# Kernel tuning notes

Hardware: AMD Instinct MI355X
Metric: run time of the kernel (lower is better)

Reference implementation:

```python
import jax, jax.numpy as jnp
import numpy as np

EPS = 1e-5

def _ln(x):
    # F.layer_norm over last dim, no affine params
    m = jnp.mean(x, axis=-1, keepdims=True)
    v = jnp.mean((x - m) ** 2, axis=-1, keepdims=True)
    return (x - m) * jax.lax.rsqrt(v + EPS)

def _jagged_to_padded(vals, offsets, B, n):
    # vals: [T, F] -> [B, n, F], zero padded
    T = vals.shape[0]
    lengths = offsets[1:] - offsets[:-1]            # [B]
    pos = jnp.arange(n)
    idx = offsets[:-1, None] + pos[None, :]         # [B, n]
    valid = pos[None, :] < lengths[:, None]         # [B, n]
    gathered = vals[jnp.clip(idx, 0, T - 1)]        # [B, n, F]
    return jnp.where(valid[..., None], gathered, 0.0)

def _dense_to_jagged(padded, offsets, T):
    # padded: [B, n, F] -> [T, F]
    t = jnp.arange(T)
    b = jnp.clip(jnp.searchsorted(offsets, t, side='right') - 1, 0, offsets.shape[0] - 2)
    pos = t - offsets[b]
    return padded[b, pos]

def setup_inputs() -> dict:
    key = jax.random.key(0)
    D, H, d = 1024, 8, 128
    B, n = 4, 2048
    T = B * n  # all sequences full length
    ks = jax.random.split(key, 4)
    x = jax.random.normal(ks[0], (T, D), dtype=jnp.float32)
    attnmask = jnp.tril(jnp.ones((n, n), dtype=jnp.float32))
    x_offsets = jnp.arange(B + 1, dtype=jnp.int32) * n
    proj_w = jax.random.normal(ks[1], (D, H * d * 4), dtype=jnp.float32) * 0.02
    out_w = jax.random.normal(ks[2], (H * d, D), dtype=jnp.float32) * 0.02
    out_b = jnp.zeros((D,), dtype=jnp.float32)
    return {"x": x, "attnmask": attnmask, "proj_w": proj_w, "out_w": out_w,
            "out_b": out_b, "x_offsets": x_offsets, "B": B, "n": n}

def reference(x, attnmask, proj_w, out_w, out_b, x_offsets, B, n):
    T, D = x.shape
    H, d4 = 8, proj_w.shape[1] // 8
    d = d4 // 4
    x = _ln(x)
    h = jax.nn.silu(x @ proj_w).reshape(T, H, 4 * d)   # silu BEFORE split (HSTU)
    u, v, q, k = jnp.split(h, 4, axis=-1)              # each [T, H, d]
    pq = _jagged_to_padded(q.reshape(T, H * d), x_offsets, B, n).reshape(B, n, H, d)
    pk = _jagged_to_padded(k.reshape(T, H * d), x_offsets, B, n).reshape(B, n, H, d)
    pv = _jagged_to_padded(v.reshape(T, H * d), x_offsets, B, n).reshape(B, n, H, d)
    scores = jnp.einsum('bnhd,bmhd->bhnm', pq, pk)
    scores = jax.nn.silu(scores) / n * attnmask[None, None]
    attnout = jnp.einsum('bhnm,bmhd->bnhd', scores, pv).reshape(B, n, H * d)
    attnout = _dense_to_jagged(attnout, x_offsets, T)  # [T, H*d]
    attnout = _ln(attnout) * u.reshape(T, H * d)       # fused norm + gate
    return attnout @ out_w + out_b                      # out_proj (dropout inactive: eval)
```

## Files before the change

### kernel.cpp

```cpp
#include <hip/hip_runtime.h>

typedef short  s16x8 __attribute__((ext_vector_type(8)));
typedef float  f32x4 __attribute__((ext_vector_type(4)));
typedef unsigned short u16;
typedef unsigned int   u32;

#define T_TOK 8192
#define D_IN  1024
#define D4    4096
#define NH    8
#define DH    128
#define NSEQ  2048

__device__ __forceinline__ float u16f(u16 s){
  union { unsigned int u; float f; } c; c.u = ((unsigned int)s) << 16; return c.f;
}
__device__ __forceinline__ u16 f2u16(float f){
  union { float f; unsigned int u; } c; c.f = f;
  unsigned int r = (c.u + 0x7fffu + ((c.u >> 16) & 1u)) >> 16;
  return (u16)r;
}
__device__ __forceinline__ unsigned int cvt2_bf16(float a, float b){
  unsigned int r;
  asm("v_cvt_pk_bf16_f32 %0, %1, %2" : "=v"(r) : "v"(a), "v"(b));
  return r;
}
__device__ __forceinline__ float fast_silu(float v){
  return v * __builtin_amdgcn_rcpf(1.0f + __expf(-v));
}
__device__ __forceinline__ void gload_lds16(const u16* g, u16* lds){
  __builtin_amdgcn_global_load_lds(
      (const __attribute__((address_space(1))) u32*)g,
      (__attribute__((address_space(3))) u32*)lds, 16, 0, 0);
}

__device__ __forceinline__ void block_reduce2(float& a, float& b){
  __shared__ float red[8];
  #pragma unroll
  for (int off = 32; off > 0; off >>= 1){
    a += __shfl_down(a, off, 64);
    b += __shfl_down(b, off, 64);
  }
  int w = threadIdx.x >> 6;
  if ((threadIdx.x & 63) == 0){ red[w*2] = a; red[w*2+1] = b; }
  __syncthreads();
  a = red[0] + red[2] + red[4] + red[6];
  b = red[1] + red[3] + red[5] + red[7];
  __syncthreads();
}

__global__ void ln_x_kernel(const float* __restrict__ x, u16* __restrict__ xn){
  int t = blockIdx.x;
  const float* row = x + (size_t)t * D_IN;
  int base = threadIdx.x * 4;
  float4 v = *(const float4*)(row + base);
  float s = v.x + v.y + v.z + v.w;
  float q = v.x*v.x + v.y*v.y + v.z*v.z + v.w*v.w;
  block_reduce2(s, q);
  float mean = s * (1.0f / D_IN);
  float var  = q * (1.0f / D_IN) - mean * mean;
  float rstd = rsqrtf(var + 1e-5f);
  ushort4 o;
  o.x = f2u16((v.x - mean) * rstd); o.y = f2u16((v.y - mean) * rstd);
  o.z = f2u16((v.z - mean) * rstd); o.w = f2u16((v.w - mean) * rstd);
  *(ushort4*)(xn + (size_t)t * D_IN + base) = o;
}

__global__ void transpose_kernel(const float* __restrict__ in, u16* __restrict__ out,
                                 int R, int C){
  __shared__ u16 tile[32][33];
  int c0 = blockIdx.x * 32, r0 = blockIdx.y * 32;
  for (int i = threadIdx.y; i < 32; i += 8)
    tile[i][threadIdx.x] = f2u16(in[(size_t)(r0 + i) * C + c0 + threadIdx.x]);
  __syncthreads();
  for (int i = threadIdx.y; i < 32; i += 8)
    out[(size_t)(c0 + i) * R + r0 + threadIdx.x] = tile[threadIdx.x][i];
}

__global__ void vt_kernel(const u16* __restrict__ h, u16* __restrict__ vt){
  __shared__ u16 tile[32][33];
  int bh = blockIdx.z; int b = bh >> 3, hh = bh & 7;
  int p0 = blockIdx.x * 32, d0 = blockIdx.y * 32;
  const u16* src = h + (size_t)(b * NSEQ) * D4 + hh * 512 + 128;
  for (int i = threadIdx.y; i < 32; i += 8)
    tile[i][threadIdx.x] = src[(size_t)(p0 + i) * D4 + d0 + threadIdx.x];
  __syncthreads();
  u16* dst = vt + (size_t)bh * DH * NSEQ;
  for (int i = threadIdx.y; i < 32; i += 8)
    dst[(size_t)(d0 + i) * NSEQ + p0 + threadIdx.x] = tile[threadIdx.x][i];
}

template<int EPI>
__global__ __launch_bounds__(256, 2) void gemm_bt_kernel(
    const u16* __restrict__ A, const u16* __restrict__ Bt,
    const float* __restrict__ bias, u16* __restrict__ Cb, float* __restrict__ Cf,
    int M, int N, int K)
{
  __shared__ __align__(16) u16 As[128 * 64];
  __shared__ __align__(16) u16 Bs[128 * 64];
  int bn = blockIdx.x, bm = blockIdx.y;
  int tid = threadIdx.x;
  int lane = tid & 63, wave = tid >> 6;
  int lr = lane & 15, quad = lane >> 4;
  int wm = (wave >> 1) * 64, wn = (wave & 1) * 64;
  f32x4 acc[4][4] = {};

  int srow = lane >> 3;
  int scol = ((lane & 7) ^ srow) * 8;
  const u16* Ab = A  + (size_t)(bm * 128) * K;
  const u16* Bb = Bt + (size_t)(bn * 128) * K;
  int swz = (lr & 7) * 8;

  for (int k0 = 0; k0 < K; k0 += 64){
    #pragma unroll
    for (int it = 0; it < 4; ++it){
      int c = it * 4 + wave;
      gload_lds16(Ab + (size_t)(c * 8 + srow) * K + k0 + scol, As + c * 512);
    }
    #pragma unroll
    for (int it = 0; it < 4; ++it){
      int c = it * 4 + wave;
      gload_lds16(Bb + (size_t)(c * 8 + srow) * K + k0 + scol, Bs + c * 512);
    }
    __syncthreads();
    #pragma unroll
    for (int ks = 0; ks < 2; ++ks){
      s16x8 af[4], bf[4];
      #pragma unroll
      for (int i = 0; i < 4; ++i)
        af[i] = *(const s16x8*)&As[(wm + i*16 + lr) * 64 + (((ks*32 + quad*8)) ^ swz)];
      #pragma unroll
      for (int j = 0; j < 4; ++j)
        bf[j] = *(const s16x8*)&Bs[(wn + j*16 + lr) * 64 + (((ks*32 + quad*8)) ^ swz)];
      #pragma unroll
      for (int i = 0; i < 4; ++i)
        #pragma unroll
        for (int j = 0; j < 4; ++j)
          acc[i][j] = __builtin_amdgcn_mfma_f32_16x16x32_bf16(af[i], bf[j], acc[i][j], 0, 0, 0);
    }
    __syncthreads();
  }
  #pragma unroll
  for (int j = 0; j < 4; ++j){
    int nc = bn * 128 + wn + j * 16 + lr;
    float bv = 0.0f;
    if (EPI == 1) bv = bias[nc];
    #pragma unroll
    for (int i = 0; i < 4; ++i){
      #pragma unroll
      for (int r = 0; r < 4; ++r){
        int mr = bm * 128 + wm + i * 16 + quad * 4 + r;
        float v = acc[i][j][r];
        if (EPI == 0){
          v = fast_silu(v);
          Cb[(size_t)mr * N + nc] = f2u16(v);
        } else {
          Cf[(size_t)mr * N + nc] = v + bv;
        }
      }
    }
  }
}

__global__ __launch_bounds__(256, 2) void attn_kernel(
    const u16* __restrict__ h, const u16* __restrict__ vt, u16* __restrict__ ao)
{
  __shared__ __align__(16) u16 smem[40960];

  int id = blockIdx.x;
  int qt, bh;
  if (id < 256) { qt = id & 15;        bh = id >> 4;          }
  else          { qt = 15 - (id & 15); bh = 16 + ((id - 256) >> 4); }
  int b = bh >> 3, hh = bh & 7;
  int tid = threadIdx.x;
  int lane = tid & 63, wave = tid >> 6;
  int lr = lane & 15, quad = lane >> 4;
  int wq = wave * 32;

  const u16* kbase = h  + (size_t)(b * NSEQ) * D4 + hh * 512 + 384;
  const u16* vbase = vt + (size_t)bh * DH * NSEQ;
  u16* Ssl = smem + 32768;

  auto stage = [&](int bufsel, int k0n){
    u16* kd = smem + bufsel * 8192;
    u16* vd = smem + 16384 + bufsel * 8192;
    #pragma unroll
    for (int it = 0; it < 4; ++it){
      int c = it * 4 + wave;
      int row = c * 4 + (lane >> 4);
      int ss = (lane & 15) ^ (row & 15);
      gload_lds16(kbase + (size_t)(k0n + row) * D4 + ss * 8, kd + c * 512);
    }
    #pragma unroll
    for (int it = 0; it < 4; ++it){
      int c = it * 4 + wave;
      int row = c * 8 + (lane >> 3);
      int ss = (lane & 7) ^ (lane >> 3);
      gload_lds16(vbase + (size_t)row * NSEQ + k0n + ss * 8, vd + c * 512);
    }
  };

  const u16* qsrc = h + (size_t)(b * NSEQ + qt * 128) * D4 + hh * 512 + 256;
  s16x8 qf[2][4];
  #pragma unroll
  for (int i = 0; i < 2; ++i)
    #pragma unroll
    for (int ks = 0; ks < 4; ++ks)
      qf[i][ks] = *(const s16x8*)(qsrc + (size_t)(wq + i*16 + lr) * D4 + ks*32 + quad*8);

  stage(0, 0);
  __syncthreads();

  f32x4 oacc[2][8] = {};
  int nkt = 2 * qt + 2;

  for (int kt = 0; kt < nkt; ++kt){
    int cur = kt & 1;
    int k0 = kt * 64;
    if (kt + 1 < nkt) stage(cur ^ 1, k0 + 64);

    const u16* kc = smem + cur * 8192;
    const u16* vc = smem + 16384 + cur * 8192;

    int lk0 = k0 - qt * 128;
    bool active = (lk0 < wq + 32);
    if (active){
      f32x4 sacc[2][4] = {};
      __builtin_amdgcn_s_setprio(1);
      #pragma unroll
      for (int ks = 0; ks < 4; ++ks){
        s16x8 kf[4];
        #pragma unroll
        for (int jb = 0; jb < 4; ++jb)
          kf[jb] = *(const s16x8*)&kc[(jb*16 + lr) * 128 + (((ks*4 + quad) ^ lr) << 3)];
        #pragma unroll
        for (int i = 0; i < 2; ++i)
          #pragma unroll
          for (int jb = 0; jb < 4; ++jb)
            sacc[i][jb] = __builtin_amdgcn_mfma_f32_16x16x32_bf16(qf[i][ks], kf[jb], sacc[i][jb], 0, 0, 0);
      }
      __builtin_amdgcn_s_setprio(0);

      bool needmask = (lk0 + 63 > wq);
      #pragma unroll
      for (int i = 0; i < 2; ++i)
        #pragma unroll
        for (int jb = 0; jb < 4; ++jb){
          int qbase = wq + i*16 + quad*4;
          int slot = jb*2 + (lr >> 3);
          int off  = lr & 7;
          float p[4];
          if (needmask){
            #pragma unroll
            for (int r = 0; r < 4; ++r){
              float v = fast_silu(sacc[i][jb][r]);
              if (lk0 + jb*16 + lr > qbase + r) v = 0.0f;
              p[r] = v;
            }
          } else {
            #pragma unroll
            for (int r = 0; r < 4; ++r)
              p[r] = fast_silu(sacc[i][jb][r]);
          }
          unsigned int c01 = cvt2_bf16(p[0], p[1]);
          unsigned int c23 = cvt2_bf16(p[2], p[3]);
          Ssl[(qbase+0)*64 + (((slot ^ ((qbase+0)&7)) << 3) | off)] = (u16)(c01);
          Ssl[(qbase+1)*64 + (((slot ^ ((qbase+1)&7)) << 3) | off)] = (u16)(c01 >> 16);
          Ssl[(qbase+2)*64 + (((slot ^ ((qbase+2)&7)) << 3) | off)] = (u16)(c23);
          Ssl[(qbase+3)*64 + (((slot ^ ((qbase+3)&7)) << 3) | off)] = (u16)(c23 >> 16);
        }

      __builtin_amdgcn_s_setprio(1);
      #pragma unroll
      for (int ks = 0; ks < 2; ++ks){
        s16x8 pf[2], vf2[8];
        #pragma unroll
        for (int i = 0; i < 2; ++i)
          pf[i] = *(const s16x8*)&Ssl[(wq + i*16 + lr) * 64 + (((ks*4 + quad) ^ (lr & 7)) << 3)];
        #pragma unroll
        for (int j = 0; j < 8; ++j)
          vf2[j] = *(const s16x8*)&vc[(j*16 + lr) * 64 + (((ks*4 + quad) ^ (lr & 7)) << 3)];
        #pragma unroll
        for (int i = 0; i < 2; ++i)
          #pragma unroll
          for (int j = 0; j < 8; ++j)
            oacc[i][j] = __builtin_amdgcn_mfma_f32_16x16x32_bf16(pf[i], vf2[j], oacc[i][j], 0, 0, 0);
      }
      __builtin_amdgcn_s_setprio(0);
    }
    __syncthreads();
  }

  u16* aobase = ao + (size_t)(b * NSEQ + qt * 128) * D_IN + hh * DH;
  #pragma unroll
  for (int i = 0; i < 2; ++i)
    #pragma unroll
    for (int j = 0; j < 8; ++j){
      float s0 = oacc[i][j][0] * (1.0f / (float)NSEQ);
      float s1 = oacc[i][j][1] * (1.0f / (float)NSEQ);
      float s2 = oacc[i][j][2] * (1.0f / (float)NSEQ);
      float s3 = oacc[i][j][3] * (1.0f / (float)NSEQ);
      unsigned int c01 = cvt2_bf16(s0, s1);
      unsigned int c23 = cvt2_bf16(s2, s3);
      int rbase = wq + i*16 + quad*4;
      aobase[(size_t)(rbase+0) * D_IN + j*16 + lr] = (u16)(c01);
      aobase[(size_t)(rbase+1) * D_IN + j*16 + lr] = (u16)(c01 >> 16);
      aobase[(size_t)(rbase+2) * D_IN + j*16 + lr] = (u16)(c23);
      aobase[(size_t)(rbase+3) * D_IN + j*16 + lr] = (u16)(c23 >> 16);
    }
}

__global__ void ln_gate_kernel(const u16* __restrict__ ao, const u16* __restrict__ h,
                               u16* __restrict__ gated){
  int t = blockIdx.x;
  const u16* row = ao + (size_t)t * D_IN;
  int base = threadIdx.x * 4;
  ushort4 raw = *(const ushort4*)(row + base);
  float vx = u16f(raw.x), vy = u16f(raw.y), vz = u16f(raw.z), vw = u16f(raw.w);
  float s = vx + vy + vz + vw;
  float q = vx*vx + vy*vy + vz*vz + vw*vw;
  block_reduce2(s, q);
  float mean = s * (1.0f / D_IN);
  float var  = q * (1.0f / D_IN) - mean * mean;
  float rstd = rsqrtf(var + 1e-5f);
  ushort4 uu = *(const ushort4*)(h + (size_t)t * D4 + (base >> 7) * 512 + (base & 127));
  ushort4 o;
  o.x = f2u16((vx - mean) * rstd * u16f(uu.x));
  o.y = f2u16((vy - mean) * rstd * u16f(uu.y));
  o.z = f2u16((vz - mean) * rstd * u16f(uu.z));
  o.w = f2u16((vw - mean) * rstd * u16f(uu.w));
  *(ushort4*)(gated + (size_t)t * D_IN + base) = o;
}

extern "C" void kernel_launch(void* const* d_in, const int* in_sizes, int n_in,
                              void* d_out, int out_size, void* d_ws, size_t ws_size,
                              hipStream_t stream)
{
  (void)in_sizes; (void)n_in; (void)out_size; (void)ws_size;
  const float* x      = (const float*)d_in[0];
  const float* proj_w = (const float*)d_in[2];
  const float* out_w  = (const float*)d_in[3];
  const float* out_b  = (const float*)d_in[4];
  float* out = (float*)d_out;

  const size_t MB = 1024 * 1024;
  char* ws = (char*)d_ws;
  u16* xn  = (u16*)(ws);
  u16* h   = (u16*)(ws + 16 * MB);
  u16* Wt  = (u16*)(ws + 80 * MB);
  u16* OWt = (u16*)(ws + 88 * MB);
  u16* Vt  = (u16*)(ws + 90 * MB);
  u16* ao    = xn;
  u16* gated = Vt;

  dim3 tb32(32, 8);
  hipLaunchKernelGGL(transpose_kernel, dim3(D4 / 32, D_IN / 32), tb32, 0, stream,
                     proj_w, Wt, D_IN, D4);
  hipLaunchKernelGGL(transpose_kernel, dim3(D_IN / 32, D_IN / 32), tb32, 0, stream,
                     out_w, OWt, D_IN, D_IN);
  hipLaunchKernelGGL(ln_x_kernel, dim3(T_TOK), dim3(256), 0, stream, x, xn);
  hipLaunchKernelGGL(HIP_KERNEL_NAME(gemm_bt_kernel<0>), dim3(D4 / 128, T_TOK / 128),
                     dim3(256), 0, stream, xn, Wt, (const float*)nullptr, h,
                     (float*)nullptr, T_TOK, D4, D_IN);
  hipLaunchKernelGGL(vt_kernel, dim3(NSEQ / 32, DH / 32, 32), tb32, 0, stream, h, Vt);
  hipLaunchKernelGGL(attn_kernel, dim3(512), dim3(256), 0, stream, h, Vt, ao);
  hipLaunchKernelGGL(ln_gate_kernel, dim3(T_TOK), dim3(256), 0, stream, ao, h, gated);
  hipLaunchKernelGGL(HIP_KERNEL_NAME(gemm_bt_kernel<1>), dim3(D_IN / 128, T_TOK / 128),
                     dim3(256), 0, stream, gated, OWt, out_b, (u16*)nullptr,
                     out, T_TOK, D_IN, D_IN);
}
```

Before: 319.4 us.

## Split attention query tile across 8 waves of 16 rows each

The attention kernel moves from 4 waves handling 32 query rows each to 8 waves (512 threads) handling 16 rows each, with cooperative K/V staging split over 8 waves. The goal is more waves resident per CU to hide latency, and finer causal skipping per wave. In exchange, each wave reuses every K/V fragment loaded from LDS for only one query row-block instead of two, which raises LDS read traffic per MFMA. Launch bounds also move to (512,4), which may limit registers.

```diff
diff --git a/kernel.cpp b/kernel.cpp
--- a/kernel.cpp
+++ b/kernel.cpp
@@ -162,7 +162,7 @@
   }
 }
 
-__global__ __launch_bounds__(256, 2) void attn_kernel(
+__global__ __launch_bounds__(512, 4) void attn_kernel(
     const u16* __restrict__ h, const u16* __restrict__ vt, u16* __restrict__ ao)
 {
   __shared__ __align__(16) u16 smem[40960];
@@ -175,7 +175,7 @@
   int tid = threadIdx.x;
   int lane = tid & 63, wave = tid >> 6;
   int lr = lane & 15, quad = lane >> 4;
-  int wq = wave * 32;
+  int wq = wave * 16;
 
   const u16* kbase = h  + (size_t)(b * NSEQ) * D4 + hh * 512 + 384;
   const u16* vbase = vt + (size_t)bh * DH * NSEQ;
@@ -185,15 +185,15 @@
     u16* kd = smem + bufsel * 8192;
     u16* vd = smem + 16384 + bufsel * 8192;
     #pragma unroll
-    for (int it = 0; it < 4; ++it){
-      int c = it * 4 + wave;
+    for (int it = 0; it < 2; ++it){
+      int c = it * 8 + wave;
       int row = c * 4 + (lane >> 4);
       int ss = (lane & 15) ^ (row & 15);
       gload_lds16(kbase + (size_t)(k0n + row) * D4 + ss * 8, kd + c * 512);
     }
     #pragma unroll
-    for (int it = 0; it < 4; ++it){
-      int c = it * 4 + wave;
+    for (int it = 0; it < 2; ++it){
+      int c = it * 8 + wave;
       int row = c * 8 + (lane >> 3);
       int ss = (lane & 7) ^ (lane >> 3);
       gload_lds16(vbase + (size_t)row * NSEQ + k0n + ss * 8, vd + c * 512);
@@ -201,17 +201,15 @@
   };
 
   const u16* qsrc = h + (size_t)(b * NSEQ + qt * 128) * D4 + hh * 512 + 256;
-  s16x8 qf[2][4];
+  s16x8 qf[4];
   #pragma unroll
-  for (int i = 0; i < 2; ++i)
-    #pragma unroll
-    for (int ks = 0; ks < 4; ++ks)
-      qf[i][ks] = *(const s16x8*)(qsrc + (size_t)(wq + i*16 + lr) * D4 + ks*32 + quad*8);
+  for (int ks = 0; ks < 4; ++ks)
+    qf[ks] = *(const s16x8*)(qsrc + (size_t)(wq + lr) * D4 + ks*32 + quad*8);
 
   stage(0, 0);
   __syncthreads();
 
-  f32x4 oacc[2][8] = {};
+  f32x4 oacc[8] = {};
   int nkt = 2 * qt + 2;
 
   for (int kt = 0; kt < nkt; ++kt){
@@ -223,9 +221,9 @@
     const u16* vc = smem + 16384 + cur * 8192;
 
     int lk0 = k0 - qt * 128;
-    bool active = (lk0 < wq + 32);
+    bool active = (lk0 < wq + 16);
     if (active){
-      f32x4 sacc[2][4] = {};
+      f32x4 sacc[4] = {};
       __builtin_amdgcn_s_setprio(1);
       #pragma unroll
       for (int ks = 0; ks < 4; ++ks){
@@ -234,57 +232,49 @@
         for (int jb = 0; jb < 4; ++jb)
           kf[jb] = *(const s16x8*)&kc[(jb*16 + lr) * 128 + (((ks*4 + quad) ^ lr) << 3)];
         #pragma unroll
-        for (int i = 0; i < 2; ++i)
-          #pragma unroll
-          for (int jb = 0; jb < 4; ++jb)
-            sacc[i][jb] = __builtin_amdgcn_mfma_f32_16x16x32_bf16(qf[i][ks], kf[jb], sacc[i][jb], 0, 0, 0);
+        for (int jb = 0; jb < 4; ++jb)
+          sacc[jb] = __builtin_amdgcn_mfma_f32_16x16x32_bf16(qf[ks], kf[jb], sacc[jb], 0, 0, 0);
       }
       __builtin_amdgcn_s_setprio(0);
 
       bool needmask = (lk0 + 63 > wq);
       #pragma unroll
-      for (int i = 0; i < 2; ++i)
-        #pragma unroll
-        for (int jb = 0; jb < 4; ++jb){
-          int qbase = wq + i*16 + quad*4;
-          int slot = jb*2 + (lr >> 3);
-          int off  = lr & 7;
-          float p[4];
-          if (needmask){
-            #pragma unroll
-            for (int r = 0; r < 4; ++r){
-              float v = fast_silu(sacc[i][jb][r]);
-              if (lk0 + jb*16 + lr > qbase + r) v = 0.0f;
-              p[r] = v;
-            }
-          } else {
-            #pragma unroll
-            for (int r = 0; r < 4; ++r)
-              p[r] = fast_silu(sacc[i][jb][r]);
+      for (int jb = 0; jb < 4; ++jb){
+        int qbase = wq + quad*4;
+        int slot = jb*2 + (lr >> 3);
+        int off  = lr & 7;
+        float p[4];
+        if (needmask){
+          #pragma unroll
+          for (int r = 0; r < 4; ++r){
+            float v = fast_silu(sacc[jb][r]);
+            if (lk0 + jb*16 + lr > qbase + r) v = 0.0f;
+            p[r] = v;
           }
-          unsigned int c01 = cvt2_bf16(p[0], p[1]);
-          unsigned int c23 = cvt2_bf16(p[2], p[3]);
-          Ssl[(qbase+0)*64 + (((slot ^ ((qbase+0)&7)) << 3) | off)] = (u16)(c01);
-          Ssl[(qbase+1)*64 + (((slot ^ ((qbase+1)&7)) << 3) | off)] = (u16)(c01 >> 16);
-          Ssl[(qbase+2)*64 + (((slot ^ ((qbase+2)&7)) << 3) | off)] = (u16)(c23);
-          Ssl[(qbase+3)*64 + (((slot ^ ((qbase+3)&7)) << 3) | off)] = (u16)(c23 >> 16);
+        } else {
+          #pragma unroll
+          for (int r = 0; r < 4; ++r)
+            p[r] = fast_silu(sacc[jb][r]);
         }
+        unsigned int c01 = cvt2_bf16(p[0], p[1]);
+        unsigned int c23 = cvt2_bf16(p[2], p[3]);
+        Ssl[(qbase+0)*64 + (((slot ^ ((qbase+0)&7)) << 3) | off)] = (u16)(c01);
+        Ssl[(qbase+1)*64 + (((slot ^ ((qbase+1)&7)) << 3) | off)] = (u16)(c01 >> 16);
+        Ssl[(qbase+2)*64 + (((slot ^ ((qbase+2)&7)) << 3) | off)] = (u16)(c23);
+        Ssl[(qbase+3)*64 + (((slot ^ ((qbase+3)&7)) << 3) | off)] = (u16)(c23 >> 16);
+      }
 
       __builtin_amdgcn_s_setprio(1);
       #pragma unroll
       for (int ks = 0; ks < 2; ++ks){
-        s16x8 pf[2], vf2[8];
-        #pragma unroll
-        for (int i = 0; i < 2; ++i)
-          pf[i] = *(const s16x8*)&Ssl[(wq + i*16 + lr) * 64 + (((ks*4 + quad) ^ (lr & 7)) << 3)];
+        s16x8 pf, vf2[8];
+        pf = *(const s16x8*)&Ssl[(wq + lr) * 64 + (((ks*4 + quad) ^ (lr & 7)) << 3)];
         #pragma unroll
         for (int j = 0; j < 8; ++j)
           vf2[j] = *(const s16x8*)&vc[(j*16 + lr) * 64 + (((ks*4 + quad) ^ (lr & 7)) << 3)];
         #pragma unroll
-        for (int i = 0; i < 2; ++i)
-          #pragma unroll
-          for (int j = 0; j < 8; ++j)
-            oacc[i][j] = __builtin_amdgcn_mfma_f32_16x16x32_bf16(pf[i], vf2[j], oacc[i][j], 0, 0, 0);
+        for (int j = 0; j < 8; ++j)
+          oacc[j] = __builtin_amdgcn_mfma_f32_16x16x32_bf16(pf, vf2[j], oacc[j], 0, 0, 0);
       }
       __builtin_amdgcn_s_setprio(0);
     }
@@ -293,21 +283,19 @@
 
   u16* aobase = ao + (size_t)(b * NSEQ + qt * 128) * D_IN + hh * DH;
   #pragma unroll
-  for (int i = 0; i < 2; ++i)
-    #pragma unroll
-    for (int j = 0; j < 8; ++j){
-      float s0 = oacc[i][j][0] * (1.0f / (float)NSEQ);
-      float s1 = oacc[i][j][1] * (1.0f / (float)NSEQ);
-      float s2 = oacc[i][j][2] * (1.0f / (float)NSEQ);
-      float s3 = oacc[i][j][3] * (1.0f / (float)NSEQ);
-      unsigned int c01 = cvt2_bf16(s0, s1);
-      unsigned int c23 = cvt2_bf16(s2, s3);
-      int rbase = wq + i*16 + quad*4;
-      aobase[(size_t)(rbase+0) * D_IN + j*16 + lr] = (u16)(c01);
-      aobase[(size_t)(rbase+1) * D_IN + j*16 + lr] = (u16)(c01 >> 16);
-      aobase[(size_t)(rbase+2) * D_IN + j*16 + lr] = (u16)(c23);
-      aobase[(size_t)(rbase+3) * D_IN + j*16 + lr] = (u16)(c23 >> 16);
-    }
+  for (int j = 0; j < 8; ++j){
+    float s0 = oacc[j][0] * (1.0f / (float)NSEQ);
+    float s1 = oacc[j][1] * (1.0f / (float)NSEQ);
+    float s2 = oacc[j][2] * (1.0f / (float)NSEQ);
+    float s3 = oacc[j][3] * (1.0f / (float)NSEQ);
+    unsigned int c01 = cvt2_bf16(s0, s1);
+    unsigned int c23 = cvt2_bf16(s2, s3);
+    int rbase = wq + quad*4;
+    aobase[(size_t)(rbase+0) * D_IN + j*16 + lr] = (u16)(c01);
+    aobase[(size_t)(rbase+1) * D_IN + j*16 + lr] = (u16)(c01 >> 16);
+    aobase[(size_t)(rbase+2) * D_IN + j*16 + lr] = (u16)(c23);
+    aobase[(size_t)(rbase+3) * D_IN + j*16 + lr] = (u16)(c23 >> 16);
+  }
 }
 
 __global__ void ln_gate_kernel(const u16* __restrict__ ao, const u16* __restrict__ h,
@@ -363,7 +351,7 @@
                      dim3(256), 0, stream, xn, Wt, (const float*)nullptr, h,
                      (float*)nullptr, T_TOK, D4, D_IN);
   hipLaunchKernelGGL(vt_kernel, dim3(NSEQ / 32, DH / 32, 32), tb32, 0, stream, h, Vt);
-  hipLaunchKernelGGL(attn_kernel, dim3(512), dim3(256), 0, stream, h, Vt, ao);
+  hipLaunchKernelGGL(attn_kernel, dim3(512), dim3(512), 0, stream, h, Vt, ao);
   hipLaunchKernelGGL(ln_gate_kernel, dim3(T_TOK), dim3(256), 0, stream, ao, h, gated);
   hipLaunchKernelGGL(HIP_KERNEL_NAME(gemm_bt_kernel<1>), dim3(D_IN / 128, T_TOK / 128),
                      dim3(256), 0, stream, gated, OWt, out_b, (u16*)nullptr,
```

Result: faster. 311.1 us (-2.6%).

## Split attention key tiles across two wave groups and reduce partial outputs

Applied to the files above, without the earlier changes.

The attention block grows to 512 threads in two groups of four waves. Each group handles alternating 64-key tiles with its own double-buffered K/V staging, and the P tile now reuses the K buffer instead of a separate slice. At the end, group 1's partial outputs go through shared memory and group 0 adds them before writing. The aim is more waves per block to hide latency and halve the serial key loop, at the cost of 128KB of LDS (lower occupancy), an extra mid-loop barrier and a final reduction.

```diff
diff --git a/kernel.cpp b/kernel.cpp
--- a/kernel.cpp
+++ b/kernel.cpp
@@ -162,10 +162,10 @@
   }
 }
 
-__global__ __launch_bounds__(256, 2) void attn_kernel(
+__global__ __launch_bounds__(512, 2) void attn_kernel(
     const u16* __restrict__ h, const u16* __restrict__ vt, u16* __restrict__ ao)
 {
-  __shared__ __align__(16) u16 smem[40960];
+  __shared__ __align__(16) u16 smem[65536];
 
   int id = blockIdx.x;
   int qt, bh;
@@ -174,26 +174,27 @@
   int b = bh >> 3, hh = bh & 7;
   int tid = threadIdx.x;
   int lane = tid & 63, wave = tid >> 6;
+  int g = wave >> 2, w4 = wave & 3;
   int lr = lane & 15, quad = lane >> 4;
-  int wq = wave * 32;
+  int wq = w4 * 32;
 
   const u16* kbase = h  + (size_t)(b * NSEQ) * D4 + hh * 512 + 384;
   const u16* vbase = vt + (size_t)bh * DH * NSEQ;
-  u16* Ssl = smem + 32768;
-
-  auto stage = [&](int bufsel, int k0n){
-    u16* kd = smem + bufsel * 8192;
-    u16* vd = smem + 16384 + bufsel * 8192;
+
+  auto stage = [&](int d, int t){
+    u16* kd = smem + (size_t)(g*2 + d) * 8192;
+    u16* vd = smem + 32768 + (size_t)(g*2 + d) * 8192;
+    int k0n = t * 64;
     #pragma unroll
     for (int it = 0; it < 4; ++it){
-      int c = it * 4 + wave;
+      int c = it * 4 + w4;
       int row = c * 4 + (lane >> 4);
       int ss = (lane & 15) ^ (row & 15);
       gload_lds16(kbase + (size_t)(k0n + row) * D4 + ss * 8, kd + c * 512);
     }
     #pragma unroll
     for (int it = 0; it < 4; ++it){
-      int c = it * 4 + wave;
+      int c = it * 4 + w4;
       int row = c * 8 + (lane >> 3);
       int ss = (lane & 7) ^ (lane >> 3);
       gload_lds16(vbase + (size_t)row * NSEQ + k0n + ss * 8, vd + c * 512);
@@ -208,24 +209,26 @@
     for (int ks = 0; ks < 4; ++ks)
       qf[i][ks] = *(const s16x8*)(qsrc + (size_t)(wq + i*16 + lr) * D4 + ks*32 + quad*8);
 
-  stage(0, 0);
+  stage(0, g);
   __syncthreads();
 
   f32x4 oacc[2][8] = {};
-  int nkt = 2 * qt + 2;
-
-  for (int kt = 0; kt < nkt; ++kt){
-    int cur = kt & 1;
-    int k0 = kt * 64;
-    if (kt + 1 < nkt) stage(cur ^ 1, k0 + 64);
-
-    const u16* kc = smem + cur * 8192;
-    const u16* vc = smem + 16384 + cur * 8192;
-
-    int lk0 = k0 - qt * 128;
+  int npair = qt + 1;
+
+  for (int s = 0; s < npair; ++s){
+    int cur = s & 1;
+    if (s + 1 < npair) stage(cur ^ 1, 2*(s+1) + g);
+
+    const u16* kc = smem + (size_t)(g*2 + cur) * 8192;
+    const u16* vc = smem + 32768 + (size_t)(g*2 + cur) * 8192;
+    u16* Ssl = (u16*)kc;
+
+    int t = 2*s + g;
+    int lk0 = t * 64 - qt * 128;
     bool active = (lk0 < wq + 32);
+
+    f32x4 sacc[2][4] = {};
     if (active){
-      f32x4 sacc[2][4] = {};
       __builtin_amdgcn_s_setprio(1);
       #pragma unroll
       for (int ks = 0; ks < 4; ++ks){
@@ -240,7 +243,11 @@
             sacc[i][jb] = __builtin_amdgcn_mfma_f32_16x16x32_bf16(qf[i][ks], kf[jb], sacc[i][jb], 0, 0, 0);
       }
       __builtin_amdgcn_s_setprio(0);
-
+    }
+    __builtin_amdgcn_s_barrier();
+    __builtin_amdgcn_sched_barrier(0);
+
+    if (active){
       bool needmask = (lk0 + 63 > wq);
       #pragma unroll
       for (int i = 0; i < 2; ++i)
@@ -291,23 +298,36 @@
     __syncthreads();
   }
 
-  u16* aobase = ao + (size_t)(b * NSEQ + qt * 128) * D_IN + hh * DH;
-  #pragma unroll
-  for (int i = 0; i < 2; ++i)
-    #pragma unroll
-    for (int j = 0; j < 8; ++j){
-      float s0 = oacc[i][j][0] * (1.0f / (float)NSEQ);
-      float s1 = oacc[i][j][1] * (1.0f / (float)NSEQ);
-      float s2 = oacc[i][j][2] * (1.0f / (float)NSEQ);
-      float s3 = oacc[i][j][3] * (1.0f / (float)NSEQ);
-      unsigned int c01 = cvt2_bf16(s0, s1);
-      unsigned int c23 = cvt2_bf16(s2, s3);
-      int rbase = wq + i*16 + quad*4;
-      aobase[(size_t)(rbase+0) * D_IN + j*16 + lr] = (u16)(c01);
-      aobase[(size_t)(rbase+1) * D_IN + j*16 + lr] = (u16)(c01 >> 16);
-      aobase[(size_t)(rbase+2) * D_IN + j*16 + lr] = (u16)(c23);
-      aobase[(size_t)(rbase+3) * D_IN + j*16 + lr] = (u16)(c23 >> 16);
-    }
+  f32x4* FV = (f32x4*)(smem + 32768);
+  if (g == 1){
+    #pragma unroll
+    for (int i = 0; i < 2; ++i)
+      #pragma unroll
+      for (int j = 0; j < 8; ++j)
+        FV[w4*1024 + (i*8 + j)*64 + lane] = oacc[i][j];
+  }
+  __syncthreads();
+  if (g == 0){
+    u16* aobase = ao + (size_t)(b * NSEQ + qt * 128) * D_IN + hh * DH;
+    #pragma unroll
+    for (int i = 0; i < 2; ++i)
+      #pragma unroll
+      for (int j = 0; j < 8; ++j){
+        f32x4 o4 = oacc[i][j];
+        f32x4 p4 = FV[w4*1024 + (i*8 + j)*64 + lane];
+        float s0 = (o4[0] + p4[0]) * (1.0f / (float)NSEQ);
+        float s1 = (o4[1] + p4[1]) * (1.0f / (float)NSEQ);
+        float s2 = (o4[2] + p4[2]) * (1.0f / (float)NSEQ);
+        float s3 = (o4[3] + p4[3]) * (1.0f / (float)NSEQ);
+        unsigned int c01 = cvt2_bf16(s0, s1);
+        unsigned int c23 = cvt2_bf16(s2, s3);
+        int rbase = wq + i*16 + quad*4;
+        aobase[(size_t)(rbase+0) * D_IN + j*16 + lr] = (u16)(c01);
+        aobase[(size_t)(rbase+1) * D_IN + j*16 + lr] = (u16)(c01 >> 16);
+        aobase[(size_t)(rbase+2) * D_IN + j*16 + lr] = (u16)(c23);
+        aobase[(size_t)(rbase+3) * D_IN + j*16 + lr] = (u16)(c23 >> 16);
+      }
+  }
 }
 
 __global__ void ln_gate_kernel(const u16* __restrict__ ao, const u16* __restrict__ h,
@@ -363,7 +383,7 @@
                      dim3(256), 0, stream, xn, Wt, (const float*)nullptr, h,
                      (float*)nullptr, T_TOK, D4, D_IN);
   hipLaunchKernelGGL(vt_kernel, dim3(NSEQ / 32, DH / 32, 32), tb32, 0, stream, h, Vt);
-  hipLaunchKernelGGL(attn_kernel, dim3(512), dim3(256), 0, stream, h, Vt, ao);
+  hipLaunchKernelGGL(attn_kernel, dim3(512), dim3(512), 0, stream, h, Vt, ao);
   hipLaunchKernelGGL(ln_gate_kernel, dim3(T_TOK), dim3(256), 0, stream, ao, h, gated);
   hipLaunchKernelGGL(HIP_KERNEL_NAME(gemm_bt_kernel<1>), dim3(D_IN / 128, T_TOK / 128),
                      dim3(256), 0, stream, gated, OWt, out_b, (u16*)nullptr,
```

Result: slower. 329.2 us (+3.1%).

## Split attention key tile across two wave groups with LDS reduction

Applied to the files above, without the earlier changes.

Doubles the attention block to 512 threads, where two groups of four waves each handle half of every 64-key tile for the same query rows. The two partial output accumulators are combined through shared memory before writing out. The aim is more waves in flight to hide latency and finer causal skipping at 32-key granularity. The cost is an extra LDS reduction, an extra barrier, and more register pressure under the new launch bounds.

```diff
diff --git a/kernel.cpp b/kernel.cpp
--- a/kernel.cpp
+++ b/kernel.cpp
@@ -162,7 +162,7 @@
   }
 }
 
-__global__ __launch_bounds__(256, 2) void attn_kernel(
+__global__ __launch_bounds__(512, 4) void attn_kernel(
     const u16* __restrict__ h, const u16* __restrict__ vt, u16* __restrict__ ao)
 {
   __shared__ __align__(16) u16 smem[40960];
@@ -174,8 +174,9 @@
   int b = bh >> 3, hh = bh & 7;
   int tid = threadIdx.x;
   int lane = tid & 63, wave = tid >> 6;
+  int kh = wave >> 2;
+  int R  = (wave & 3) * 32;
   int lr = lane & 15, quad = lane >> 4;
-  int wq = wave * 32;
 
   const u16* kbase = h  + (size_t)(b * NSEQ) * D4 + hh * 512 + 384;
   const u16* vbase = vt + (size_t)bh * DH * NSEQ;
@@ -185,15 +186,15 @@
     u16* kd = smem + bufsel * 8192;
     u16* vd = smem + 16384 + bufsel * 8192;
     #pragma unroll
-    for (int it = 0; it < 4; ++it){
-      int c = it * 4 + wave;
+    for (int it = 0; it < 2; ++it){
+      int c = it * 8 + wave;
       int row = c * 4 + (lane >> 4);
       int ss = (lane & 15) ^ (row & 15);
       gload_lds16(kbase + (size_t)(k0n + row) * D4 + ss * 8, kd + c * 512);
     }
     #pragma unroll
-    for (int it = 0; it < 4; ++it){
-      int c = it * 4 + wave;
+    for (int it = 0; it < 2; ++it){
+      int c = it * 8 + wave;
       int row = c * 8 + (lane >> 3);
       int ss = (lane & 7) ^ (lane >> 3);
       gload_lds16(vbase + (size_t)row * NSEQ + k0n + ss * 8, vd + c * 512);
@@ -206,7 +207,7 @@
   for (int i = 0; i < 2; ++i)
     #pragma unroll
     for (int ks = 0; ks < 4; ++ks)
-      qf[i][ks] = *(const s16x8*)(qsrc + (size_t)(wq + i*16 + lr) * D4 + ks*32 + quad*8);
+      qf[i][ks] = *(const s16x8*)(qsrc + (size_t)(R + i*16 + lr) * D4 + ks*32 + quad*8);
 
   stage(0, 0);
   __syncthreads();
@@ -223,38 +224,39 @@
     const u16* vc = smem + 16384 + cur * 8192;
 
     int lk0 = k0 - qt * 128;
-    bool active = (lk0 < wq + 32);
+    int kb0 = lk0 + kh * 32;
+    bool active = (kb0 < R + 32);
     if (active){
-      f32x4 sacc[2][4] = {};
+      f32x4 sacc[2][2] = {};
       __builtin_amdgcn_s_setprio(1);
       #pragma unroll
       for (int ks = 0; ks < 4; ++ks){
-        s16x8 kf[4];
-        #pragma unroll
-        for (int jb = 0; jb < 4; ++jb)
-          kf[jb] = *(const s16x8*)&kc[(jb*16 + lr) * 128 + (((ks*4 + quad) ^ lr) << 3)];
+        s16x8 kf[2];
+        #pragma unroll
+        for (int jb = 0; jb < 2; ++jb)
+          kf[jb] = *(const s16x8*)&kc[(kh*32 + jb*16 + lr) * 128 + (((ks*4 + quad) ^ lr) << 3)];
         #pragma unroll
         for (int i = 0; i < 2; ++i)
           #pragma unroll
-          for (int jb = 0; jb < 4; ++jb)
+          for (int jb = 0; jb < 2; ++jb)
             sacc[i][jb] = __builtin_amdgcn_mfma_f32_16x16x32_bf16(qf[i][ks], kf[jb], sacc[i][jb], 0, 0, 0);
       }
       __builtin_amdgcn_s_setprio(0);
 
-      bool needmask = (lk0 + 63 > wq);
+      bool needmask = (kb0 + 31 > R);
       #pragma unroll
       for (int i = 0; i < 2; ++i)
         #pragma unroll
-        for (int jb = 0; jb < 4; ++jb){
-          int qbase = wq + i*16 + quad*4;
-          int slot = jb*2 + (lr >> 3);
+        for (int jb = 0; jb < 2; ++jb){
+          int qbase = R + i*16 + quad*4;
+          int slot = kh*4 + jb*2 + (lr >> 3);
           int off  = lr & 7;
           float p[4];
           if (needmask){
             #pragma unroll
             for (int r = 0; r < 4; ++r){
               float v = fast_silu(sacc[i][jb][r]);
-              if (lk0 + jb*16 + lr > qbase + r) v = 0.0f;
+              if (kb0 + jb*16 + lr > qbase + r) v = 0.0f;
               p[r] = v;
             }
           } else {
@@ -271,15 +273,14 @@
         }
 
       __builtin_amdgcn_s_setprio(1);
-      #pragma unroll
-      for (int ks = 0; ks < 2; ++ks){
+      {
         s16x8 pf[2], vf2[8];
         #pragma unroll
         for (int i = 0; i < 2; ++i)
-          pf[i] = *(const s16x8*)&Ssl[(wq + i*16 + lr) * 64 + (((ks*4 + quad) ^ (lr & 7)) << 3)];
+          pf[i] = *(const s16x8*)&Ssl[(R + i*16 + lr) * 64 + (((kh*4 + quad) ^ (lr & 7)) << 3)];
         #pragma unroll
         for (int j = 0; j < 8; ++j)
-          vf2[j] = *(const s16x8*)&vc[(j*16 + lr) * 64 + (((ks*4 + quad) ^ (lr & 7)) << 3)];
+          vf2[j] = *(const s16x8*)&vc[(j*16 + lr) * 64 + (((kh*4 + quad) ^ (lr & 7)) << 3)];
         #pragma unroll
         for (int i = 0; i < 2; ++i)
           #pragma unroll
@@ -291,23 +292,36 @@
     __syncthreads();
   }
 
-  u16* aobase = ao + (size_t)(b * NSEQ + qt * 128) * D_IN + hh * DH;
-  #pragma unroll
-  for (int i = 0; i < 2; ++i)
-    #pragma unroll
-    for (int j = 0; j < 8; ++j){
-      float s0 = oacc[i][j][0] * (1.0f / (float)NSEQ);
-      float s1 = oacc[i][j][1] * (1.0f / (float)NSEQ);
-      float s2 = oacc[i][j][2] * (1.0f / (float)NSEQ);
-      float s3 = oacc[i][j][3] * (1.0f / (float)NSEQ);
-      unsigned int c01 = cvt2_bf16(s0, s1);
-      unsigned int c23 = cvt2_bf16(s2, s3);
-      int rbase = wq + i*16 + quad*4;
-      aobase[(size_t)(rbase+0) * D_IN + j*16 + lr] = (u16)(c01);
-      aobase[(size_t)(rbase+1) * D_IN + j*16 + lr] = (u16)(c01 >> 16);
-      aobase[(size_t)(rbase+2) * D_IN + j*16 + lr] = (u16)(c23);
-      aobase[(size_t)(rbase+3) * D_IN + j*16 + lr] = (u16)(c23 >> 16);
-    }
+  f32x4* FV = (f32x4*)smem;
+  if (kh == 1){
+    #pragma unroll
+    for (int i = 0; i < 2; ++i)
+      #pragma unroll
+      for (int j = 0; j < 8; ++j)
+        FV[(wave - 4)*1024 + (i*8 + j)*64 + lane] = oacc[i][j];
+  }
+  __syncthreads();
+  if (kh == 0){
+    u16* aobase = ao + (size_t)(b * NSEQ + qt * 128) * D_IN + hh * DH;
+    #pragma unroll
+    for (int i = 0; i < 2; ++i)
+      #pragma unroll
+      for (int j = 0; j < 8; ++j){
+        f32x4 o4 = oacc[i][j];
+        f32x4 p4 = FV[wave*1024 + (i*8 + j)*64 + lane];
+        float s0 = (o4[0] + p4[0]) * (1.0f / (float)NSEQ);
+        float s1 = (o4[1] + p4[1]) * (1.0f / (float)NSEQ);
+        float s2 = (o4[2] + p4[2]) * (1.0f / (float)NSEQ);
+        float s3 = (o4[3] + p4[3]) * (1.0f / (float)NSEQ);
+        unsigned int c01 = cvt2_bf16(s0, s1);
+        unsigned int c23 = cvt2_bf16(s2, s3);
+        int rbase = R + i*16 + quad*4;
+        aobase[(size_t)(rbase+0) * D_IN + j*16 + lr] = (u16)(c01);
+        aobase[(size_t)(rbase+1) * D_IN + j*16 + lr] = (u16)(c01 >> 16);
+        aobase[(size_t)(rbase+2) * D_IN + j*16 + lr] = (u16)(c23);
+        aobase[(size_t)(rbase+3) * D_IN + j*16 + lr] = (u16)(c23 >> 16);
+      }
+  }
 }
 
 __global__ void ln_gate_kernel(const u16* __restrict__ ao, const u16* __restrict__ h,
@@ -363,7 +377,7 @@
                      dim3(256), 0, stream, xn, Wt, (const float*)nullptr, h,
                      (float*)nullptr, T_TOK, D4, D_IN);
   hipLaunchKernelGGL(vt_kernel, dim3(NSEQ / 32, DH / 32, 32), tb32, 0, stream, h, Vt);
-  hipLaunchKernelGGL(attn_kernel, dim3(512), dim3(256), 0, stream, h, Vt, ao);
+  hipLaunchKernelGGL(attn_kernel, dim3(512), dim3(512), 0, stream, h, Vt, ao);
   hipLaunchKernelGGL(ln_gate_kernel, dim3(T_TOK), dim3(256), 0, stream, ao, h, gated);
   hipLaunchKernelGGL(HIP_KERNEL_NAME(gemm_bt_kernel<1>), dim3(D_IN / 128, T_TOK / 128),
                      dim3(256), 0, stream, gated, OWt, out_b, (u16*)nullptr,
```

New measurement: 563.1 us. +76.3%, slower.
